# Kernel optimization log

Hardware: AMD Instinct MI355X
Metric: run time of the kernel (lower is better)

## Reference

```python
import jax, jax.numpy as jnp
from jax import lax
import numpy as np

LOGZERO = -1e10  # matches the repo's `logzero` sentinel


def setup_inputs() -> dict:
    key = jax.random.key(0)
    k1, k2, k3, k4 = jax.random.split(key, 4)
    bs, xmax, vocab, ymax = 32, 1024, 1000, 128
    # CTC log-probabilities (ctc_generator output is log_softmax in the repo)
    ctc_out = jax.nn.log_softmax(
        jax.random.normal(k1, (bs, xmax, vocab), jnp.float32), axis=-1)
    src_size = jax.random.randint(k2, (bs,), xmax // 2, xmax + 1)
    src_mask = (jnp.arange(xmax)[None, :] < src_size[:, None])[:, None, :]  # [bs,1,xmax] bool
    ys = jax.random.randint(k3, (bs, ymax), 1, vocab)   # non-blank labels
    ylens = jax.random.randint(k4, (bs,), ymax // 2, ymax + 1)
    return {"ctc_out": ctc_out, "src_mask": src_mask, "src_size": src_size,
            "ys": ys, "ylens": ylens, "blank": 0}


def reference(ctc_out, src_mask, src_size, ys, ylens, blank):
    bs, xmax, vocab = ctc_out.shape
    ymax = ys.shape[1]
    L = 2 * ymax + 1  # blank-interleaved path length

    # mask invalid frames to logzero (masked_fill in torch)
    lp = jnp.where(src_mask.transpose(0, 2, 1), ctc_out, LOGZERO)  # [bs,xmax,vocab]

    # blank-interleaved path: [blank, y1, blank, y2, ..., blank]
    path = jnp.full((bs, L), blank, dtype=ys.dtype).at[:, 1::2].set(ys)
    path_lens = 2 * ylens + 1

    # log-probs gathered along the path: [xmax, bs, L] (time-major for scan)
    lp_path = jnp.take_along_axis(
        lp, jnp.broadcast_to(path[:, None, :], (bs, xmax, L)), axis=2)
    lp_path = lp_path.transpose(1, 0, 2)

    same_tr = path[:, :-2] == path[:, 2:]                 # [bs, L-2]
    idx = jnp.arange(L)
    outside = idx[None, :] >= path_lens[:, None]          # [bs, L]

    alpha0 = jnp.full((bs, L), LOGZERO, jnp.float32).at[:, 0].set(0.0)

    def step(alpha, lp_t):
        m0 = alpha
        m1 = jnp.concatenate([jnp.full((bs, 1), LOGZERO, alpha.dtype), alpha[:, :-1]], axis=1)
        m2 = jnp.concatenate([jnp.full((bs, 2), LOGZERO, alpha.dtype),
                              jnp.where(same_tr, LOGZERO, alpha[:, :-2])], axis=1)
        mat = jnp.stack([m0, m1, m2])                     # [3, bs, L]
        max_prob = jnp.max(mat, axis=0)
        arg = jnp.argmax(mat, axis=0)
        bp_t = idx[None, :] - arg                          # back-pointer (path position)
        max_prob = jnp.where(outside, LOGZERO, max_prob)
        alpha_new = max_prob + lp_t
        return alpha_new, (alpha_new, bp_t)

    _, (alpha_hist, bp) = lax.scan(step, alpha0, lp_path)  # [xmax,bs,L] each
    alpha_full = jnp.concatenate([alpha0[None], alpha_hist], axis=0)  # [xmax+1,bs,L]

    b_idx = jnp.arange(bs)
    alpha_at = alpha_full[src_size, b_idx]                 # [bs, L] alpha at t = src_size
    s1 = alpha_at[b_idx, path_lens - 1]
    s2 = alpha_at[b_idx, path_lens - 2]
    start = jnp.where(s1 > s2, path_lens - 1, path_lens - 2)
    score = jnp.maximum(s1, s2)                            # best alignment log-prob per utt

    # vectorized backtrace over all batches (reverse scan over time)
    def back_step(carry, t):
        tt = jnp.minimum(t + 1, xmax - 1)
        prev = bp[tt, b_idx, carry]                        # bp[b, t+1, state_{t+1}]
        val = jnp.where(t == src_size - 1, start,
                        jnp.where(t < src_size - 1, prev, 0))
        return val, val

    ts = jnp.arange(xmax - 1, -1, -1)
    _, states_rev = lax.scan(back_step, jnp.zeros((bs,), start.dtype), ts)
    states = states_rev[::-1].T                            # [bs, xmax] path positions

    aligned = jnp.take_along_axis(path, states, axis=1)    # [bs, xmax] tokens
    shift = jnp.concatenate([jnp.zeros((bs, 1), aligned.dtype), aligned[:, :-1]], axis=1)
    aligned = jnp.where(aligned == shift, 0, aligned)      # collapse repeats to 0
    shift2 = jnp.concatenate([jnp.zeros((bs, 1), aligned.dtype), aligned[:, :-1]], axis=1)

    csum = jnp.cumsum((shift2 != blank).astype(jnp.int32), axis=1)  # [bs, xmax]
    tm = csum[:, None, :] == jnp.arange(ymax + 1)[None, :, None]    # [bs, ymax+1, xmax]
    last = tm[:, -1, :] & src_mask[:, 0, :]
    last = last.at[b_idx, src_size - 1].set(True)
    tm = tm.at[:, -1, :].set(last)
    trigger_mask = tm & src_mask                           # & x_mask from FaNat.forward

    return score, trigger_mask, ylens + 1
```

## Files before the change

### kernel.cpp

```cpp
#include <hip/hip_runtime.h>
#include <stdint.h>

#define LOGZERO (-1e10f)

static constexpr int BS    = 32;
static constexpr int XMAX  = 1024;
static constexpr int VOCAB = 1000;
static constexpr int YMAX  = 128;
static constexpr int NROWS = YMAX + 1;
static constexpr int CH    = 8;
static constexpr int NPROD = 8;
static constexpr int NWAVES = 1 + NPROD;
static constexpr int NPAIR = XMAX / 2;
static constexpr size_t LPWS_BYTES = (size_t)BS * XMAX * 256 * 4;

__global__ __launch_bounds__(256) void k_gather(
    const float* __restrict__ ctc, const int* __restrict__ src_size,
    const int* __restrict__ ys, const int* __restrict__ blankp,
    float* __restrict__ lp_ws)
{
    const int blk  = blockIdx.x;
    const int b    = blk >> 4;
    const int seg  = blk & 15;
    const int wid  = threadIdx.x >> 6;
    const int lane = threadIdx.x & 63;
    const int ss   = src_size[b];
    const int bv   = blankp[0];
    const int tokA = ys[b * YMAX + 2 * lane];
    const int tokB = ys[b * YMAX + 2 * lane + 1];
    const float* baseg = ctc + (size_t)b * XMAX * VOCAB;
    float* basew = lp_ws + (size_t)b * XMAX * 256 + lane * 4;
    const int t0 = seg * 64 + wid * 16;
    #pragma unroll 4
    for (int r = 0; r < 16; ++r) {
        const int t = t0 + r;
        if (t < ss) {
            const float* rp = baseg + (size_t)t * VOCAB;
            float vb = rp[bv], va = rp[tokA], vc = rp[tokB];
            *reinterpret_cast<float4*>(basew + (size_t)t * 256) =
                make_float4(vb, va, vb, vc);
        }
    }
}

template<bool STAGED>
__global__ __launch_bounds__(64 * NWAVES) void k_viterbi(
    const float* __restrict__ ctc, const float* __restrict__ lp_ws,
    const int* __restrict__ src_size,
    const int* __restrict__ ys, const int* __restrict__ ylens,
    const int* __restrict__ blankp, int* __restrict__ csum_ws,
    float* __restrict__ out)
{
    __shared__ float buf[2][CH][256];
    __shared__ unsigned char  bpb[XMAX * 64];
    __shared__ unsigned char  g4pack[XMAX / CH];
    __shared__ unsigned short bp2[NPAIR * 64];
    __shared__ unsigned char  bp2_256[NPAIR];
    __shared__ unsigned short st_lds[XMAX];
    __shared__ int ysl[YMAX];

    const int b    = blockIdx.x;
    const int tid  = threadIdx.x;
    const int wid  = tid >> 6;
    const int lane = tid & 63;
    const int ss   = src_size[b];
    const int yl   = ylens[b];
    const int bv   = blankp[0];
    const int plen = 2 * yl + 1;
    const float LZ = LOGZERO;

    for (int j = tid; j < YMAX; j += 64 * NWAVES) ysl[j] = ys[b * YMAX + j];
    for (int t = tid; t < XMAX; t += 64 * NWAVES) st_lds[t] = 0;
    __syncthreads();

    const int nchunk = (ss + CH - 1) / CH;
    const float* baseg = ctc + (size_t)b * XMAX * VOCAB;

    int start = 0;

    if (wid == 0) {
        const int tokA = ysl[2 * lane];
        const int tokB = ysl[2 * lane + 1];
        const bool al1 = (lane > 0) && (tokA != ysl[2 * lane - 1]);
        const bool al3 = (tokB != tokA);
        const bool o0 = (4 * lane     >= plen);
        const bool o1 = (4 * lane + 1 >= plen);
        const bool o2 = (4 * lane + 2 >= plen);
        const bool o3 = (4 * lane + 3 >= plen);
        const bool o4 = (256 >= plen);
        const int rotidx = (lane + 63) & 63;

        float a0 = (lane == 0) ? 0.0f : LZ;
        float a1 = LZ, a2 = LZ, a3 = LZ, a4 = LZ;
        float rotp = __shfl(a3, rotidx);

        for (int c = 0; c < nchunk; ++c) {
            __builtin_amdgcn_s_barrier();
            asm volatile("" ::: "memory");
            __builtin_amdgcn_sched_barrier(0);
            const int cb = c & 1;
            float4 q[CH];
            #pragma unroll
            for (int r = 0; r < CH; ++r)
                q[r] = *reinterpret_cast<const float4*>(&buf[cb][r][lane * 4]);
            unsigned int g4acc = 0;
            #pragma unroll
            for (int r = 0; r < CH; ++r) {
                const int t = c * CH + r;
                if (t < ss) {
                    float m3 = a3; int g3 = 0;
                    if (a2 > m3) { m3 = a2; g3 = 1; }
                    float sk3 = al3 ? a1 : LZ;
                    if (sk3 > m3) { m3 = sk3; g3 = 2; }
                    float a3n = (o3 ? LZ : m3) + q[r].w;
                    float rot = rotp;
                    rotp = __shfl(a3n, rotidx);
                    float p3 = (lane == 0) ? LZ : rot;
                    float m0 = a0; int g0 = 0; if (p3 > m0) { m0 = p3; g0 = 1; }
                    float m1 = a1; int g1 = 0; if (a0 > m1) { m1 = a0; g1 = 1; }
                    float sk1 = al1 ? p3 : LZ;  if (sk1 > m1) { m1 = sk1; g1 = 2; }
                    float m2 = a2; int g2 = 0; if (a1 > m2) { m2 = a1; g2 = 1; }
                    float m4 = a4; int g4 = 0; if (rot > m4) { m4 = rot; g4 = 1; }
                    a0 = (o0 ? LZ : m0) + q[r].x;
                    a1 = (o1 ? LZ : m1) + q[r].y;
                    a2 = (o2 ? LZ : m2) + q[r].z;
                    a3 = a3n;
                    a4 = (o4 ? LZ : m4) + q[r].x;
                    g4acc |= (unsigned)g4 << r;
                    bpb[t * 64 + lane] =
                        (unsigned char)(g0 | (g1 << 2) | (g2 << 4) | (g3 << 6));
                }
            }
            if (lane == 0) g4pack[c] = (unsigned char)g4acc;
        }

        auto getA = [&](int idx) -> float {
            if (idx == 256) return __shfl(a4, 0);
            int k = idx & 3;
            float pick = (k == 0) ? a0 : (k == 1) ? a1 : (k == 2) ? a2 : a3;
            return __shfl(pick, idx >> 2);
        };
        const float s1v = getA(plen - 1), s2v = getA(plen - 2);
        const float score = (s1v > s2v) ? s1v : s2v;
        start = (s1v > s2v) ? (plen - 1) : (plen - 2);
        if (lane == 0) {
            out[b] = score;
            out[32 + (size_t)BS * NROWS * XMAX + b] = (float)(yl + 1);
        }
    } else if (STAGED) {
        const int pr = wid - 1;
        const float* basew = lp_ws + (size_t)b * XMAX * 256 + lane * 4;
        float4 v0 = *reinterpret_cast<const float4*>(basew + (size_t)pr * 256);
        float4 v1 = *reinterpret_cast<const float4*>(basew + (size_t)(CH + pr) * 256);
        for (int c = 0; c < nchunk; ++c) {
            if (c & 1) {
                *reinterpret_cast<float4*>(&buf[1][pr][lane * 4]) = v1;
                int tn = (c + 2) * CH + pr; if (tn > XMAX - 1) tn = XMAX - 1;
                v1 = *reinterpret_cast<const float4*>(basew + (size_t)tn * 256);
            } else {
                *reinterpret_cast<float4*>(&buf[0][pr][lane * 4]) = v0;
                int tn = (c + 2) * CH + pr; if (tn > XMAX - 1) tn = XMAX - 1;
                v0 = *reinterpret_cast<const float4*>(basew + (size_t)tn * 256);
            }
            asm volatile("s_waitcnt lgkmcnt(0)" ::: "memory");
            __builtin_amdgcn_s_barrier();
        }
    } else {
        const int pr = wid - 1;
        const int tokA = ysl[2 * lane];
        const int tokB = ysl[2 * lane + 1];
        int t0 = pr; if (t0 >= ss) t0 = ss - 1;
        const float* r0 = baseg + (size_t)t0 * VOCAB;
        float vb0 = r0[bv], va0 = r0[tokA], vc0 = r0[tokB];
        int t1 = CH + pr; if (t1 >= ss) t1 = ss - 1;
        const float* r1 = baseg + (size_t)t1 * VOCAB;
        float vb1 = r1[bv], va1 = r1[tokA], vc1 = r1[tokB];
        for (int c = 0; c < nchunk; ++c) {
            if (c & 1) {
                *reinterpret_cast<float4*>(&buf[1][pr][lane * 4]) =
                    make_float4(vb1, va1, vb1, vc1);
                int tn = (c + 2) * CH + pr; if (tn >= ss) tn = ss - 1;
                const float* r = baseg + (size_t)tn * VOCAB;
                vb1 = r[bv]; va1 = r[tokA]; vc1 = r[tokB];
            } else {
                *reinterpret_cast<float4*>(&buf[0][pr][lane * 4]) =
                    make_float4(vb0, va0, vb0, vc0);
                int tn = (c + 2) * CH + pr; if (tn >= ss) tn = ss - 1;
                const float* r = baseg + (size_t)tn * VOCAB;
                vb0 = r[bv]; va0 = r[tokA]; vc0 = r[tokB];
            }
            asm volatile("s_waitcnt lgkmcnt(0)" ::: "memory");
            __builtin_amdgcn_s_barrier();
        }
    }
    __syncthreads();

    const int pmax = (ss - 1) >> 1;
    for (int p = 1 + wid; p <= pmax; p += NWAVES) {
        int oOdd  = bpb[(2 * p + 1) * 64 + lane];
        int oEven = bpb[(2 * p) * 64 + lane];
        int uEven = (lane > 0) ? bpb[(2 * p) * 64 + lane - 1] : 0;
        int evenWin = uEven | (oEven << 8);
        unsigned int acc = 0;
        #pragma unroll
        for (int k = 0; k < 4; ++k) {
            int a1v = (oOdd >> (2 * k)) & 3;
            int sh  = 2 * k - 2 * a1v + 8;
            int a2v = (evenWin >> sh) & 3;
            acc |= (unsigned)(a1v | (a2v << 2)) << (4 * k);
        }
        bp2[p * 64 + lane] = (unsigned short)acc;
        const int tOdd = 2 * p + 1, tEven = 2 * p;
        int a16 = (g4pack[tOdd >> 3] >> (tOdd & 7)) & 1;
        int a26 = (a16 == 0) ? ((g4pack[tEven >> 3] >> (tEven & 7)) & 1)
                             : ((bpb[tEven * 64 + 63] >> 6) & 3);
        if (lane == 0) bp2_256[p] = (unsigned char)(a16 | (a26 << 2));
    }
    __syncthreads();

    if (tid == 0) {
        int s = start, tc = ss - 1;
        st_lds[tc] = (unsigned short)s;
        if ((tc & 1) == 0 && tc >= 1) {
            int arg;
            if (s == 256) arg = (g4pack[tc >> 3] >> (tc & 7)) & 1;
            else arg = (bpb[tc * 64 + (s >> 2)] >> ((s & 3) * 2)) & 3;
            s -= arg; --tc; st_lds[tc] = (unsigned short)s;
        }
        while (tc > 1) {
            int n;
            if (s == 256) n = bp2_256[tc >> 1];
            else n = (bp2[(tc >> 1) * 64 + (s >> 2)] >> ((s & 3) * 4)) & 0xF;
            int sA = s - (n & 3);
            int sB = sA - (n >> 2);
            st_lds[tc - 1] = (unsigned short)sA;
            st_lds[tc - 2] = (unsigned short)sB;
            s = sB; tc -= 2;
        }
        if (tc == 1) {
            int arg;
            if (s == 256) arg = (g4pack[0] >> 1) & 1;
            else arg = (bpb[64 + (s >> 2)] >> ((s & 3) * 2)) & 3;
            s -= arg; st_lds[0] = (unsigned short)s;
        }
    }
    __syncthreads();

    if (wid == 0) {
        auto tok_lds = [&](int stv) -> int { return (stv & 1) ? ysl[stv >> 1] : bv; };
        const int t0c = lane * 16;
        int prev_raw = (t0c == 0) ? 0 : tok_lds(st_lds[t0c - 1]);
        int cnt = 0;
        int csl[16];
        #pragma unroll
        for (int i = 0; i < 16; ++i) {
            int raw = tok_lds(st_lds[t0c + i]);
            int ac = (raw == prev_raw) ? 0 : raw;
            prev_raw = raw;
            csl[i] = cnt;
            cnt += (ac != bv) ? 1 : 0;
        }
        int v = cnt;
        #pragma unroll
        for (int off = 1; off < 64; off <<= 1) {
            int u = __shfl_up(v, off);
            if (lane >= off) v += u;
        }
        const int base_c = v - cnt;
        int* co = csum_ws + b * XMAX + t0c;
        #pragma unroll
        for (int i = 0; i < 16; ++i) co[i] = base_c + csl[i];
    }
}

__global__ __launch_bounds__(256) void k_mask(
    const int* __restrict__ csum_ws, const int* __restrict__ src_size,
    float* __restrict__ out)
{
    int bj = blockIdx.x;
    int b = bj / NROWS, j = bj - b * NROWS;
    int ss = src_size[b];
    const int* cs = csum_ws + b * XMAX;
    float* orow = out + 32 + (size_t)bj * XMAX;
    int t = threadIdx.x * 4;
    float4 v;
    float* vp = &v.x;
    #pragma unroll
    for (int i = 0; i < 4; ++i) {
        int tt = t + i;
        int c = cs[tt];
        bool in = tt < ss;
        bool val;
        if (j < YMAX) val = (c == j) && in;
        else          val = ((c == YMAX) || (tt == ss - 1)) && in;
        vp[i] = val ? 1.0f : 0.0f;
    }
    *(float4*)(orow + t) = v;
}

extern "C" void kernel_launch(void* const* d_in, const int* in_sizes, int n_in,
                              void* d_out, int out_size, void* d_ws, size_t ws_size,
                              hipStream_t stream) {
    const float* ctc      = (const float*)d_in[0];
    const int*   src_size = (const int*)d_in[2];
    const int*   ys       = (const int*)d_in[3];
    const int*   ylens    = (const int*)d_in[4];
    const int*   blankp   = (const int*)d_in[5];
    float* out = (float*)d_out;

    const size_t need = LPWS_BYTES + (size_t)BS * XMAX * sizeof(int);
    if (ws_size >= need) {
        float* lp_ws   = (float*)d_ws;
        int*   csum_ws = (int*)((char*)d_ws + LPWS_BYTES);
        k_gather<<<BS * 16, 256, 0, stream>>>(ctc, src_size, ys, blankp, lp_ws);
        k_viterbi<true><<<BS, 64 * NWAVES, 0, stream>>>(
            ctc, lp_ws, src_size, ys, ylens, blankp, csum_ws, out);
        k_mask<<<BS * NROWS, 256, 0, stream>>>(csum_ws, src_size, out);
    } else {
        int* csum_ws = (int*)d_ws;
        k_viterbi<false><<<BS, 64 * NWAVES, 0, stream>>>(
            ctc, nullptr, src_size, ys, ylens, blankp, csum_ws, out);
        k_mask<<<BS * NROWS, 256, 0, stream>>>(csum_ws, src_size, out);
    }
}
```

Before: 393.5 us.

## Use DPP lane rotation, packed 32-bit backpointers, and deeper prefetch in Viterbi

Replaces the cross-lane __shfl (ds_bpermute) in the serial Viterbi recurrence with a DPP row rotation, which removes an LDS round trip from the critical dependency chain. It also drops the per-state outside masks. Backpointer bytes for four consecutive frames are now packed into one 32-bit LDS word, so each 8-frame chunk is written with two dword stores instead of eight byte stores. The remainder chunk is peeled so the main loop needs no per-step bound checks, and the staged producer waves prefetch four chunks ahead instead of two. The DPP row rotate may only rotate within 16-lane rows rather than across the full wave, and removing the outside masks changes semantics, so correctness is a risk.

```diff
diff --git a/kernel.cpp b/kernel.cpp
--- a/kernel.cpp
+++ b/kernel.cpp
@@ -13,6 +13,12 @@
 static constexpr int NWAVES = 1 + NPROD;
 static constexpr int NPAIR = XMAX / 2;
 static constexpr size_t LPWS_BYTES = (size_t)BS * XMAX * 256 * 4;
+
+__device__ __forceinline__ float rot1(float x) {
+    int r = __builtin_amdgcn_update_dpp(0, __float_as_int(x),
+                                        0x13C , 0xF, 0xF, false);
+    return __int_as_float(r);
+}
 
 __global__ __launch_bounds__(256) void k_gather(
     const float* __restrict__ ctc, const int* __restrict__ src_size,
@@ -43,6 +49,26 @@
     }
 }
 
+#define VSTEP(qq, PK, SHIFT, RBIT) do {                                     \
+    float rot = rot1(a3);                       \
+    float p3  = (lane == 0) ? LZ : rot;                                     \
+    float sk3 = al3 ? a1 : LZ;                                              \
+    float m3 = a3; int g3 = 0;                                              \
+    if (a2  > m3) { m3 = a2;  g3 = 1; }                                     \
+    if (sk3 > m3) { m3 = sk3; g3 = 2; }                                     \
+    float sk1 = al1 ? p3 : LZ;                                              \
+    float m1 = a1; int g1 = 0;                                              \
+    if (a0  > m1) { m1 = a0;  g1 = 1; }                                     \
+    if (sk1 > m1) { m1 = sk1; g1 = 2; }                                     \
+    float m0 = a0; int g0 = 0; if (p3  > m0) { m0 = p3;  g0 = 1; }          \
+    float m2 = a2; int g2 = 0; if (a1  > m2) { m2 = a1;  g2 = 1; }          \
+    float m4 = a4; int g4 = 0; if (rot > m4) { m4 = rot; g4 = 1; }          \
+    a0 = m0 + (qq).x; a1 = m1 + (qq).y; a2 = m2 + (qq).z; a3 = m3 + (qq).w; \
+    a4 = m4 + (qq).x;                           \
+    PK |= (unsigned)(g0 | (g1 << 2) | (g2 << 4) | (g3 << 6)) << (SHIFT);    \
+    g4acc |= (unsigned)g4 << (RBIT);                                        \
+} while (0)
+
 template<bool STAGED>
 __global__ __launch_bounds__(64 * NWAVES) void k_viterbi(
     const float* __restrict__ ctc, const float* __restrict__ lp_ws,
@@ -52,7 +78,7 @@
     float* __restrict__ out)
 {
     __shared__ float buf[2][CH][256];
-    __shared__ unsigned char  bpb[XMAX * 64];
+    __shared__ unsigned int  bpb32[(XMAX / 4) * 64];
     __shared__ unsigned char  g4pack[XMAX / CH];
     __shared__ unsigned short bp2[NPAIR * 64];
     __shared__ unsigned char  bp2_256[NPAIR];
@@ -83,18 +109,14 @@
         const int tokB = ysl[2 * lane + 1];
         const bool al1 = (lane > 0) && (tokA != ysl[2 * lane - 1]);
         const bool al3 = (tokB != tokA);
-        const bool o0 = (4 * lane     >= plen);
-        const bool o1 = (4 * lane + 1 >= plen);
-        const bool o2 = (4 * lane + 2 >= plen);
-        const bool o3 = (4 * lane + 3 >= plen);
-        const bool o4 = (256 >= plen);
-        const int rotidx = (lane + 63) & 63;
 
         float a0 = (lane == 0) ? 0.0f : LZ;
         float a1 = LZ, a2 = LZ, a3 = LZ, a4 = LZ;
-        float rotp = __shfl(a3, rotidx);
-
-        for (int c = 0; c < nchunk; ++c) {
+
+        const int nfull = ss >> 3;
+        const int mrem  = ss & 7;
+
+        for (int c = 0; c < nfull; ++c) {
             __builtin_amdgcn_s_barrier();
             asm volatile("" ::: "memory");
             __builtin_amdgcn_sched_barrier(0);
@@ -103,35 +125,34 @@
             #pragma unroll
             for (int r = 0; r < CH; ++r)
                 q[r] = *reinterpret_cast<const float4*>(&buf[cb][r][lane * 4]);
-            unsigned int g4acc = 0;
-            #pragma unroll
-            for (int r = 0; r < CH; ++r) {
-                const int t = c * CH + r;
-                if (t < ss) {
-                    float m3 = a3; int g3 = 0;
-                    if (a2 > m3) { m3 = a2; g3 = 1; }
-                    float sk3 = al3 ? a1 : LZ;
-                    if (sk3 > m3) { m3 = sk3; g3 = 2; }
-                    float a3n = (o3 ? LZ : m3) + q[r].w;
-                    float rot = rotp;
-                    rotp = __shfl(a3n, rotidx);
-                    float p3 = (lane == 0) ? LZ : rot;
-                    float m0 = a0; int g0 = 0; if (p3 > m0) { m0 = p3; g0 = 1; }
-                    float m1 = a1; int g1 = 0; if (a0 > m1) { m1 = a0; g1 = 1; }
-                    float sk1 = al1 ? p3 : LZ;  if (sk1 > m1) { m1 = sk1; g1 = 2; }
-                    float m2 = a2; int g2 = 0; if (a1 > m2) { m2 = a1; g2 = 1; }
-                    float m4 = a4; int g4 = 0; if (rot > m4) { m4 = rot; g4 = 1; }
-                    a0 = (o0 ? LZ : m0) + q[r].x;
-                    a1 = (o1 ? LZ : m1) + q[r].y;
-                    a2 = (o2 ? LZ : m2) + q[r].z;
-                    a3 = a3n;
-                    a4 = (o4 ? LZ : m4) + q[r].x;
-                    g4acc |= (unsigned)g4 << r;
-                    bpb[t * 64 + lane] =
-                        (unsigned char)(g0 | (g1 << 2) | (g2 << 4) | (g3 << 6));
-                }
-            }
+            unsigned int pkA = 0, pkB = 0, g4acc = 0;
+            #pragma unroll
+            for (int r = 0; r < 4; ++r) VSTEP(q[r], pkA, r * 8, r);
+            #pragma unroll
+            for (int r = 4; r < 8; ++r) VSTEP(q[r], pkB, (r - 4) * 8, r);
+            bpb32[(2 * c) * 64 + lane]     = pkA;
+            bpb32[(2 * c + 1) * 64 + lane] = pkB;
             if (lane == 0) g4pack[c] = (unsigned char)g4acc;
+        }
+        if (mrem) {
+            __builtin_amdgcn_s_barrier();
+            asm volatile("" ::: "memory");
+            __builtin_amdgcn_sched_barrier(0);
+            const int cb = nfull & 1;
+            float4 q[CH];
+            #pragma unroll
+            for (int r = 0; r < CH; ++r)
+                q[r] = *reinterpret_cast<const float4*>(&buf[cb][r][lane * 4]);
+            unsigned int pkA = 0, pkB = 0, g4acc = 0;
+            #pragma unroll
+            for (int r = 0; r < 4; ++r)
+                if (r < mrem) VSTEP(q[r], pkA, r * 8, r);
+            #pragma unroll
+            for (int r = 4; r < 8; ++r)
+                if (r < mrem) VSTEP(q[r], pkB, (r - 4) * 8, r);
+            bpb32[(2 * nfull) * 64 + lane] = pkA;
+            if (mrem > 4) bpb32[(2 * nfull + 1) * 64 + lane] = pkB;
+            if (lane == 0) g4pack[nfull] = (unsigned char)g4acc;
         }
 
         auto getA = [&](int idx) -> float {
@@ -150,20 +171,33 @@
     } else if (STAGED) {
         const int pr = wid - 1;
         const float* basew = lp_ws + (size_t)b * XMAX * 256 + lane * 4;
-        float4 v0 = *reinterpret_cast<const float4*>(basew + (size_t)pr * 256);
-        float4 v1 = *reinterpret_cast<const float4*>(basew + (size_t)(CH + pr) * 256);
-        for (int c = 0; c < nchunk; ++c) {
-            if (c & 1) {
-                *reinterpret_cast<float4*>(&buf[1][pr][lane * 4]) = v1;
-                int tn = (c + 2) * CH + pr; if (tn > XMAX - 1) tn = XMAX - 1;
-                v1 = *reinterpret_cast<const float4*>(basew + (size_t)tn * 256);
-            } else {
-                *reinterpret_cast<float4*>(&buf[0][pr][lane * 4]) = v0;
-                int tn = (c + 2) * CH + pr; if (tn > XMAX - 1) tn = XMAX - 1;
-                v0 = *reinterpret_cast<const float4*>(basew + (size_t)tn * 256);
-            }
-            asm volatile("s_waitcnt lgkmcnt(0)" ::: "memory");
-            __builtin_amdgcn_s_barrier();
+        auto ldrow = [&](int cc) -> float4 {
+            int tn = cc * CH + pr; if (tn > XMAX - 1) tn = XMAX - 1;
+            return *reinterpret_cast<const float4*>(basew + (size_t)tn * 256);
+        };
+        float4 v0 = ldrow(0), v1 = ldrow(1), v2 = ldrow(2), v3 = ldrow(3);
+        int c = 0;
+        for (;;) {
+            *reinterpret_cast<float4*>(&buf[c & 1][pr][lane * 4]) = v0;
+            v0 = ldrow(c + 4);
+            asm volatile("s_waitcnt lgkmcnt(0)" ::: "memory");
+            __builtin_amdgcn_s_barrier();
+            if (++c >= nchunk) break;
+            *reinterpret_cast<float4*>(&buf[c & 1][pr][lane * 4]) = v1;
+            v1 = ldrow(c + 4);
+            asm volatile("s_waitcnt lgkmcnt(0)" ::: "memory");
+            __builtin_amdgcn_s_barrier();
+            if (++c >= nchunk) break;
+            *reinterpret_cast<float4*>(&buf[c & 1][pr][lane * 4]) = v2;
+            v2 = ldrow(c + 4);
+            asm volatile("s_waitcnt lgkmcnt(0)" ::: "memory");
+            __builtin_amdgcn_s_barrier();
+            if (++c >= nchunk) break;
+            *reinterpret_cast<float4*>(&buf[c & 1][pr][lane * 4]) = v3;
+            v3 = ldrow(c + 4);
+            asm volatile("s_waitcnt lgkmcnt(0)" ::: "memory");
+            __builtin_amdgcn_s_barrier();
+            if (++c >= nchunk) break;
         }
     } else {
         const int pr = wid - 1;
@@ -195,11 +229,14 @@
     }
     __syncthreads();
 
+    const unsigned char* bpb8 = reinterpret_cast<const unsigned char*>(bpb32);
+    #define BPBYTE(t, l) ((int)bpb8[(((t) >> 2) * 64 + (l)) * 4 + ((t) & 3)])
+
     const int pmax = (ss - 1) >> 1;
     for (int p = 1 + wid; p <= pmax; p += NWAVES) {
-        int oOdd  = bpb[(2 * p + 1) * 64 + lane];
-        int oEven = bpb[(2 * p) * 64 + lane];
-        int uEven = (lane > 0) ? bpb[(2 * p) * 64 + lane - 1] : 0;
+        int oOdd  = BPBYTE(2 * p + 1, lane);
+        int oEven = BPBYTE(2 * p, lane);
+        int uEven = (lane > 0) ? BPBYTE(2 * p, lane - 1) : 0;
         int evenWin = uEven | (oEven << 8);
         unsigned int acc = 0;
         #pragma unroll
@@ -213,7 +250,7 @@
         const int tOdd = 2 * p + 1, tEven = 2 * p;
         int a16 = (g4pack[tOdd >> 3] >> (tOdd & 7)) & 1;
         int a26 = (a16 == 0) ? ((g4pack[tEven >> 3] >> (tEven & 7)) & 1)
-                             : ((bpb[tEven * 64 + 63] >> 6) & 3);
+                             : ((BPBYTE(tEven, 63) >> 6) & 3);
         if (lane == 0) bp2_256[p] = (unsigned char)(a16 | (a26 << 2));
     }
     __syncthreads();
@@ -224,7 +261,7 @@
         if ((tc & 1) == 0 && tc >= 1) {
             int arg;
             if (s == 256) arg = (g4pack[tc >> 3] >> (tc & 7)) & 1;
-            else arg = (bpb[tc * 64 + (s >> 2)] >> ((s & 3) * 2)) & 3;
+            else arg = (BPBYTE(tc, s >> 2) >> ((s & 3) * 2)) & 3;
             s -= arg; --tc; st_lds[tc] = (unsigned short)s;
         }
         while (tc > 1) {
@@ -240,10 +277,11 @@
         if (tc == 1) {
             int arg;
             if (s == 256) arg = (g4pack[0] >> 1) & 1;
-            else arg = (bpb[64 + (s >> 2)] >> ((s & 3) * 2)) & 3;
+            else arg = (BPBYTE(1, s >> 2) >> ((s & 3) * 2)) & 3;
             s -= arg; st_lds[0] = (unsigned short)s;
         }
     }
+    #undef BPBYTE
     __syncthreads();
 
     if (wid == 0) {
```

Measured after the change: 357.1 us. -9.3%, faster.
